# Optimization experiments

Measured on AMD Instinct MI355X. Metric: run time of the kernel, lower is better.

The kernel has to match this reference:

```python
import jax, jax.numpy as jnp
from jax import lax
import numpy as np


def tropical_conv1d(x, w, padding, mode):
    """Tropical semiring conv1d.
    y[b,o,t] = sum_c reduce_k ( x[b,c,t+k] + w[o,c,k] )
    where reduce is min (min-plus) or max (max-plus). Zero padding like nn.Conv1d.
    x: [B, C, L], w: [O, C, K] -> y: [B, O, L + 2p - K + 1]
    """
    if padding:
        x = jnp.pad(x, ((0, 0), (0, 0), (padding, padding)))
    B, C, L = x.shape
    O, _, K = w.shape
    Lo = L - K + 1
    big = jnp.array(np.inf if mode == 'min' else -np.inf, dtype=x.dtype)
    acc0 = jnp.full((B, O, C, Lo), big, dtype=x.dtype)
    red = jnp.minimum if mode == 'min' else jnp.maximum
    wk_all = jnp.moveaxis(w, 2, 0)          # [K, O, C]
    ks = jnp.arange(K)

    def step(acc, inp):
        k, wk = inp
        xs = lax.dynamic_slice_in_dim(x, k, Lo, axis=2)      # [B, C, Lo]
        v = xs[:, None, :, :] + wk[None, :, :, None]          # [B, O, C, Lo]
        return red(acc, v), None

    acc, _ = lax.scan(step, acc0, (ks, wk_all))
    return acc.sum(axis=2)                                    # [B, O, Lo]


def avg_pool1d_2(x):
    # avg_pool1d(kernel=2, stride=2), truncating odd tail like torch
    B, C, L = x.shape
    Lh = L // 2
    return x[..., : Lh * 2].reshape(B, C, Lh, 2).mean(axis=-1)


def setup_inputs() -> dict:
    key = jax.random.key(0)
    ks = jax.random.split(key, 9)
    B, Cin, L = 64, 3, 8192
    linear_size = 32448
    s = lambda k, shape, fan: jax.random.normal(k, shape, dtype=jnp.float32) * (1.0 / np.sqrt(fan))
    return {
        'input': jax.random.normal(ks[0], (B, Cin, L), dtype=jnp.float32),
        'w1': s(ks[1], (6, Cin, 80), Cin * 80),
        'w2': s(ks[2], (16, 6, 3), 6 * 3),
        'fc1_w': s(ks[3], (120, linear_size), linear_size),
        'fc1_b': jnp.zeros((120,), jnp.float32),
        'fc2_w': s(ks[4], (84, 120), 120),
        'fc2_b': jnp.zeros((84,), jnp.float32),
        'fc3_w': s(ks[5], (10, 84), 84),
        'fc3_b': jnp.zeros((10,), jnp.float32),
    }


def reference(input, w1, w2, fc1_w, fc1_b, fc2_w, fc2_b, fc3_w, fc3_b):
    x = tropical_conv1d(input, w1, padding=2, mode='min')   # [B,6,L-75]
    x = avg_pool1d_2(x)
    x = tropical_conv1d(x, w2, padding=0, mode='max')       # [B,16,L2]
    x = avg_pool1d_2(x)
    x = x.reshape(x.shape[0], -1)                            # [B, 16*floor(L2/2)]
    x = jax.nn.relu(x @ fc1_w.T + fc1_b)
    x = jax.nn.relu(x @ fc2_w.T + fc2_b)
    return x @ fc3_w.T + fc3_b
```

## Files before the change

### kernel.cpp

```cpp
#include <hip/hip_runtime.h>

#define BB 64
#define C1 3
#define LIN 8192
#define PAD1 2
#define O1 6
#define KK1 80
#define LP1 4058

#define O2 16
#define KK2 3
#define LP2 2028

#define NFLAT 32448
#define H1 120
#define H2 84
#define NOUT 10

typedef _Float16 h2 __attribute__((ext_vector_type(2)));
typedef _Float16 f16x8 __attribute__((ext_vector_type(8)));
typedef float f32x4 __attribute__((ext_vector_type(4)));
#define BIGH ((_Float16)30000.0f)

__global__ __launch_bounds__(256) void k_prep(const float* __restrict__ w1,
                                              float* __restrict__ whb) {
  const int idx = threadIdx.x + blockIdx.x * 256;
  if (idx >= (O1 * C1) * (KK1 / 2)) return;
  const int oc = idx / (KK1 / 2);
  const int m  = idx - oc * (KK1 / 2);
  h2 v;
  v.x = (_Float16)w1[oc * KK1 + 2 * m];
  v.y = (_Float16)w1[oc * KK1 + 2 * m + 1];
  whb[idx] = __builtin_bit_cast(float, v);
}

#define TJ1 256
#define NT1 16
#define DW1 298

__global__ __launch_bounds__(256) void k_conv1(const float* __restrict__ x,
                                               const float* __restrict__ whb,
                                               float* __restrict__ p1) {
  __shared__ float AB[C1][2 * DW1 + 2];
  const int b    = blockIdx.x >> 4;
  const int tile = blockIdx.x & 15;
  const int j0   = tile * TJ1;
  const int T0   = 2 * j0;
  const int tid  = threadIdx.x;

  for (int q = tid; q < C1 * DW1; q += 256) {
    const int c = q / DW1;
    const int d = q - c * DW1;
    const int E = T0 + 2 * d - PAD1;
    const float* xc = x + ((size_t)b * C1 + c) * LIN;
    float f0 = 0.f, f1 = 0.f, f2 = 0.f;
    if ((unsigned)E < LIN) f0 = xc[E];
    if ((unsigned)(E + 1) < LIN) f1 = xc[E + 1];
    if ((unsigned)(E + 2) < LIN) f2 = xc[E + 2];
    h2 A; A.x = (_Float16)f0; A.y = (_Float16)f1;
    h2 Bv; Bv.x = (_Float16)f1; Bv.y = (_Float16)f2;
    AB[c][2 * d]     = __builtin_bit_cast(float, A);
    AB[c][2 * d + 1] = __builtin_bit_cast(float, Bv);
  }
  __syncthreads();

  const int jj = tid;
  const int j  = j0 + jj;

  float s0 = 0.f, s1 = 0.f, s2 = 0.f, s3 = 0.f, s4 = 0.f, s5 = 0.f;

#pragma unroll
  for (int c = 0; c < C1; ++c) {
    h2 aA[O1], aB[O1];
#pragma unroll
    for (int o = 0; o < O1; ++o) {
      aA[o].x = BIGH; aA[o].y = BIGH;
      aB[o].x = BIGH; aB[o].y = BIGH;
    }
#pragma unroll 4
    for (int m = 0; m < KK1 / 2; ++m) {
      float2 v = *(const float2*)&AB[c][2 * (jj + m)];
      h2 Ad = __builtin_bit_cast(h2, v.x);
      h2 Bd = __builtin_bit_cast(h2, v.y);
#pragma unroll
      for (int o = 0; o < O1; ++o) {
        h2 W = __builtin_bit_cast(h2, whb[(o * C1 + c) * (KK1 / 2) + m]);
        aA[o] = __builtin_elementwise_min(aA[o], Ad + W);
        aB[o] = __builtin_elementwise_min(aB[o], Bd + W);
      }
    }
    float r[O1];
#pragma unroll
    for (int o = 0; o < O1; ++o)
      r[o] = fminf((float)aA[o].x, (float)aA[o].y) + fminf((float)aB[o].x, (float)aB[o].y);
    s0 += r[0]; s1 += r[1]; s2 += r[2]; s3 += r[3]; s4 += r[4]; s5 += r[5];
  }
  if (j < LP1) {
    float* pb = p1 + (size_t)b * O1 * LP1 + j;
    pb[0 * LP1] = 0.5f * s0;
    pb[1 * LP1] = 0.5f * s1;
    pb[2 * LP1] = 0.5f * s2;
    pb[3 * LP1] = 0.5f * s3;
    pb[4 * LP1] = 0.5f * s4;
    pb[5 * LP1] = 0.5f * s5;
  }
}

#define T2 256
#define XT2 516

__global__ __launch_bounds__(256) void k_conv2(const float* __restrict__ p1,
                                               const float* __restrict__ w2,
                                               _Float16* __restrict__ p2h) {
  __shared__ float ps[O1][XT2];
  __shared__ float w2s[O2 * O1 * KK2];
  const int b    = blockIdx.x >> 3;
  const int tile = blockIdx.x & 7;
  const int j0   = tile * T2;
  const int tid  = threadIdx.x;

  for (int idx = tid; idx < O2 * O1 * KK2; idx += 256) w2s[idx] = w2[idx];
  for (int idx = tid; idx < O1 * XT2; idx += 256) {
    int c = idx / XT2;
    int p = idx - c * XT2;
    int t = 2 * j0 + p;
    ps[c][p] = (t < LP1) ? p1[((size_t)b * O1 + c) * LP1 + t] : 0.f;
  }
  __syncthreads();

  const int j = j0 + tid;
  if (j >= LP2) return;
  const int lb = 2 * tid;
  float xv[O1][4];
#pragma unroll
  for (int c = 0; c < O1; ++c) {
    xv[c][0] = ps[c][lb];     xv[c][1] = ps[c][lb + 1];
    xv[c][2] = ps[c][lb + 2]; xv[c][3] = ps[c][lb + 3];
  }
#pragma unroll
  for (int o = 0; o < O2; ++o) {
    float s = 0.f;
#pragma unroll
    for (int c = 0; c < O1; ++c) {
      float w0  = w2s[(o * O1 + c) * KK2 + 0];
      float w1v = w2s[(o * O1 + c) * KK2 + 1];
      float w2v = w2s[(o * O1 + c) * KK2 + 2];
      float m0 = fmaxf(fmaxf(xv[c][0] + w0, xv[c][1] + w1v), xv[c][2] + w2v);
      float m1 = fmaxf(fmaxf(xv[c][1] + w0, xv[c][2] + w1v), xv[c][3] + w2v);
      s += m0 + m1;
    }
    p2h[(size_t)b * NFLAT + o * LP2 + j] = (_Float16)(0.5f * s);
  }
}

#define KC2 64
#define NKC2 507

__global__ __launch_bounds__(256) void k_fc1(const _Float16* __restrict__ p2h,
                                             const float* __restrict__ w,
                                             _Float16* __restrict__ part) {
  __shared__ _Float16 bs[64][KC2];
  const int kc  = blockIdx.x;
  const int k0  = kc * KC2;
  const int tid = threadIdx.x;

#pragma unroll
  for (int r = 0; r < 2; ++r) {
    const int task = tid + 256 * r;
    const int row  = task >> 3;
    const int c4   = task & 7;
    float4 v = *(const float4*)&p2h[(size_t)row * NFLAT + k0 + c4 * 8];
    *(float4*)&bs[row][c4 * 8] = v;
  }
  __syncthreads();

  const int lane = tid & 63;
  const int wid  = tid >> 6;
  const int m_l  = lane & 15;
  const int q    = lane >> 4;
  const int m0   = wid * 32;

  const int rowA0 = m0 + m_l;
  int rowA1 = m0 + 16 + m_l;
  if (rowA1 > H1 - 1) rowA1 = H1 - 1;
  const float* wp0 = w + (size_t)rowA0 * NFLAT + k0 + q * 8;
  const float* wp1 = w + (size_t)rowA1 * NFLAT + k0 + q * 8;

  f32x4 acc[2][4];
#pragma unroll
  for (int t = 0; t < 2; ++t)
#pragma unroll
    for (int nt = 0; nt < 4; ++nt) acc[t][nt] = (f32x4){0.f, 0.f, 0.f, 0.f};

#pragma unroll
  for (int ks = 0; ks < 2; ++ks) {
    float4 a0l = *(const float4*)(wp0 + ks * 32);
    float4 a0h = *(const float4*)(wp0 + ks * 32 + 4);
    float4 a1l = *(const float4*)(wp1 + ks * 32);
    float4 a1h = *(const float4*)(wp1 + ks * 32 + 4);
    f16x8 A0, A1;
    A0[0] = (_Float16)a0l.x; A0[1] = (_Float16)a0l.y;
    A0[2] = (_Float16)a0l.z; A0[3] = (_Float16)a0l.w;
    A0[4] = (_Float16)a0h.x; A0[5] = (_Float16)a0h.y;
    A0[6] = (_Float16)a0h.z; A0[7] = (_Float16)a0h.w;
    A1[0] = (_Float16)a1l.x; A1[1] = (_Float16)a1l.y;
    A1[2] = (_Float16)a1l.z; A1[3] = (_Float16)a1l.w;
    A1[4] = (_Float16)a1h.x; A1[5] = (_Float16)a1h.y;
    A1[6] = (_Float16)a1h.z; A1[7] = (_Float16)a1h.w;
#pragma unroll
    for (int nt = 0; nt < 4; ++nt) {
      f16x8 Bf = *(const f16x8*)&bs[nt * 16 + m_l][ks * 32 + q * 8];
      acc[0][nt] = __builtin_amdgcn_mfma_f32_16x16x32_f16(A0, Bf, acc[0][nt], 0, 0, 0);
      acc[1][nt] = __builtin_amdgcn_mfma_f32_16x16x32_f16(A1, Bf, acc[1][nt], 0, 0, 0);
    }
  }

#pragma unroll
  for (int t = 0; t < 2; ++t)
#pragma unroll
    for (int nt = 0; nt < 4; ++nt)
#pragma unroll
      for (int r = 0; r < 4; ++r) {
        const int i = m0 + t * 16 + q * 4 + r;
        if (i < H1)
          part[((size_t)kc * H1 + i) * 64 + nt * 16 + m_l] = (_Float16)acc[t][nt][r];
      }
}

__global__ __launch_bounds__(512) void k_fc1red(const _Float16* __restrict__ part,
                                                float* __restrict__ part2) {
  __shared__ float red[512];
  const int bx  = blockIdx.x;
  const int s   = bx / H1;
  const int i   = bx - s * H1;
  const int tid = threadIdx.x;
  const int b   = tid & 63;
  const int sub = tid >> 6;
  const int kc0 = s * 127;
  const int kc1 = (kc0 + 127 < NKC2) ? kc0 + 127 : NKC2;
  float acc = 0.f;
  for (int kc = kc0 + sub; kc < kc1; kc += 8)
    acc += (float)part[((size_t)kc * H1 + i) * 64 + b];
  red[tid] = acc;
  __syncthreads();
  if (tid < 64) {
    float t = 0.f;
#pragma unroll
    for (int s2 = 0; s2 < 8; ++s2) t += red[b + 64 * s2];
    part2[((size_t)s * H1 + i) * 64 + b] = t;
  }
}

__global__ __launch_bounds__(128) void k_head(const float* __restrict__ part2,
                                              const float* __restrict__ fc1_b,
                                              const float* __restrict__ fc2_w,
                                              const float* __restrict__ fc2_b,
                                              const float* __restrict__ fc3_w,
                                              const float* __restrict__ fc3_b,
                                              float* __restrict__ out) {
  __shared__ float h1s[H1];
  __shared__ float h2s[H2];
  const int b = blockIdx.x;
  const int tid = threadIdx.x;
  if (tid < H1) {
    float v = part2[((size_t)0 * H1 + tid) * 64 + b]
            + part2[((size_t)1 * H1 + tid) * 64 + b]
            + part2[((size_t)2 * H1 + tid) * 64 + b]
            + part2[((size_t)3 * H1 + tid) * 64 + b];
    h1s[tid] = fmaxf(v + fc1_b[tid], 0.f);
  }
  __syncthreads();
  if (tid < H2) {
    float s = fc2_b[tid];
#pragma unroll 4
    for (int n = 0; n < H1; ++n) s += h1s[n] * fc2_w[tid * H1 + n];
    h2s[tid] = fmaxf(s, 0.f);
  }
  __syncthreads();
  if (tid < NOUT) {
    float s = fc3_b[tid];
#pragma unroll 4
    for (int n = 0; n < H2; ++n) s += h2s[n] * fc3_w[tid * H2 + n];
    out[b * NOUT + tid] = s;
  }
}

extern "C" void kernel_launch(void* const* d_in, const int* in_sizes, int n_in,
                              void* d_out, int out_size, void* d_ws, size_t ws_size,
                              hipStream_t stream) {
  const float* x     = (const float*)d_in[0];
  const float* w1    = (const float*)d_in[1];
  const float* w2    = (const float*)d_in[2];
  const float* fc1_w = (const float*)d_in[3];
  const float* fc1_b = (const float*)d_in[4];
  const float* fc2_w = (const float*)d_in[5];
  const float* fc2_b = (const float*)d_in[6];
  const float* fc3_w = (const float*)d_in[7];
  const float* fc3_b = (const float*)d_in[8];

  float* ws = (float*)d_ws;
  float*     p1    = ws;
  _Float16*  p2h   = (_Float16*)(p1 + (size_t)BB * O1 * LP1);
  _Float16*  part  = p2h + (size_t)BB * NFLAT;
  float*     part2 = (float*)(part + (size_t)NKC2 * H1 * 64);
  float*     whb   = part2 + (size_t)4 * H1 * 64;
  float*     out   = (float*)d_out;

  hipLaunchKernelGGL(k_prep, dim3(3), dim3(256), 0, stream, w1, whb);
  hipLaunchKernelGGL(k_conv1, dim3(BB * NT1), dim3(256), 0, stream, x, whb, p1);
  hipLaunchKernelGGL(k_conv2, dim3(BB * 8), dim3(256), 0, stream, p1, w2, p2h);
  hipLaunchKernelGGL(k_fc1, dim3(NKC2), dim3(256), 0, stream, p2h, fc1_w, part);
  hipLaunchKernelGGL(k_fc1red, dim3(4 * H1), dim3(512), 0, stream, part, part2);
  hipLaunchKernelGGL(k_head, dim3(BB), dim3(128), 0, stream, part2, fc1_b, fc2_w, fc2_b,
                     fc3_w, fc3_b, out);
}
```

Measured before the change: 144.0 us.

## Register-block conv1 to two outputs per thread with shared-memory weights

The first tropical conv kernel doubles its tile so each thread computes two output positions 256 apart. Each weight fetch is now reused across both positions, and the weights are staged in shared memory and read as float4. The input window is split into separate A/B shared arrays so four taps can be loaded with one vector read. In exchange the grid has half as many blocks and register pressure is higher, and the float4 LDS reads use thread-dependent offsets that may not be 16-byte aligned.

```diff
diff --git a/kernel.cpp b/kernel.cpp
--- a/kernel.cpp
+++ b/kernel.cpp
@@ -21,6 +21,8 @@
 typedef _Float16 f16x8 __attribute__((ext_vector_type(8)));
 typedef float f32x4 __attribute__((ext_vector_type(4)));
 #define BIGH ((_Float16)30000.0f)
+
+__device__ __forceinline__ h2 bch2(float f) { return __builtin_bit_cast(h2, f); }
 
 __global__ __launch_bounds__(256) void k_prep(const float* __restrict__ w1,
                                               float* __restrict__ whb) {
@@ -34,24 +36,27 @@
   whb[idx] = __builtin_bit_cast(float, v);
 }
 
-#define TJ1 256
-#define NT1 16
-#define DW1 298
+#define TJ1 512
+#define NT1 8
+#define DWIN 552
+#define DPAD 556
 
 __global__ __launch_bounds__(256) void k_conv1(const float* __restrict__ x,
                                                const float* __restrict__ whb,
                                                float* __restrict__ p1) {
-  __shared__ float AB[C1][2 * DW1 + 2];
-  const int b    = blockIdx.x >> 4;
-  const int tile = blockIdx.x & 15;
+  __shared__ float As[C1][DPAD];
+  __shared__ float Bs[C1][DPAD];
+  __shared__ float ws[O1 * C1 * 40];
+  const int b    = blockIdx.x >> 3;
+  const int tile = blockIdx.x & 7;
   const int j0   = tile * TJ1;
-  const int T0   = 2 * j0;
   const int tid  = threadIdx.x;
 
-  for (int q = tid; q < C1 * DW1; q += 256) {
-    const int c = q / DW1;
-    const int d = q - c * DW1;
-    const int E = T0 + 2 * d - PAD1;
+  for (int idx = tid; idx < O1 * C1 * 40; idx += 256) ws[idx] = whb[idx];
+  for (int q = tid; q < C1 * DWIN; q += 256) {
+    const int c = q / DWIN;
+    const int d = q - c * DWIN;
+    const int E = 2 * (j0 + d) - PAD1;
     const float* xc = x + ((size_t)b * C1 + c) * LIN;
     float f0 = 0.f, f1 = 0.f, f2 = 0.f;
     if ((unsigned)E < LIN) f0 = xc[E];
@@ -59,50 +64,74 @@
     if ((unsigned)(E + 2) < LIN) f2 = xc[E + 2];
     h2 A; A.x = (_Float16)f0; A.y = (_Float16)f1;
     h2 Bv; Bv.x = (_Float16)f1; Bv.y = (_Float16)f2;
-    AB[c][2 * d]     = __builtin_bit_cast(float, A);
-    AB[c][2 * d + 1] = __builtin_bit_cast(float, Bv);
+    As[c][d] = __builtin_bit_cast(float, A);
+    Bs[c][d] = __builtin_bit_cast(float, Bv);
   }
   __syncthreads();
 
   const int jj = tid;
-  const int j  = j0 + jj;
-
-  float s0 = 0.f, s1 = 0.f, s2 = 0.f, s3 = 0.f, s4 = 0.f, s5 = 0.f;
-
-#pragma unroll
+  float r1[O1] = {0.f, 0.f, 0.f, 0.f, 0.f, 0.f};
+  float r2[O1] = {0.f, 0.f, 0.f, 0.f, 0.f, 0.f};
+
   for (int c = 0; c < C1; ++c) {
-    h2 aA[O1], aB[O1];
+    h2 a1A[O1], a1B[O1], a2A[O1], a2B[O1];
 #pragma unroll
     for (int o = 0; o < O1; ++o) {
-      aA[o].x = BIGH; aA[o].y = BIGH;
-      aB[o].x = BIGH; aB[o].y = BIGH;
-    }
-#pragma unroll 4
-    for (int m = 0; m < KK1 / 2; ++m) {
-      float2 v = *(const float2*)&AB[c][2 * (jj + m)];
-      h2 Ad = __builtin_bit_cast(h2, v.x);
-      h2 Bd = __builtin_bit_cast(h2, v.y);
+      a1A[o].x = BIGH; a1A[o].y = BIGH;  a1B[o].x = BIGH; a1B[o].y = BIGH;
+      a2A[o].x = BIGH; a2A[o].y = BIGH;  a2B[o].x = BIGH; a2B[o].y = BIGH;
+    }
+#pragma unroll 2
+    for (int mq = 0; mq < 10; ++mq) {
+      float4 xa1 = *(const float4*)&As[c][jj + 4 * mq];
+      float4 xb1 = *(const float4*)&Bs[c][jj + 4 * mq];
+      float4 xa2 = *(const float4*)&As[c][jj + 256 + 4 * mq];
+      float4 xb2 = *(const float4*)&Bs[c][jj + 256 + 4 * mq];
+      h2 A10 = bch2(xa1.x), A11 = bch2(xa1.y), A12 = bch2(xa1.z), A13 = bch2(xa1.w);
+      h2 B10 = bch2(xb1.x), B11 = bch2(xb1.y), B12 = bch2(xb1.z), B13 = bch2(xb1.w);
+      h2 A20 = bch2(xa2.x), A21 = bch2(xa2.y), A22 = bch2(xa2.z), A23 = bch2(xa2.w);
+      h2 B20 = bch2(xb2.x), B21 = bch2(xb2.y), B22 = bch2(xb2.z), B23 = bch2(xb2.w);
 #pragma unroll
       for (int o = 0; o < O1; ++o) {
-        h2 W = __builtin_bit_cast(h2, whb[(o * C1 + c) * (KK1 / 2) + m]);
-        aA[o] = __builtin_elementwise_min(aA[o], Ad + W);
-        aB[o] = __builtin_elementwise_min(aB[o], Bd + W);
+        float4 wq = *(const float4*)&ws[(o * C1 + c) * 40 + 4 * mq];
+        h2 w0 = bch2(wq.x), w1v = bch2(wq.y), w2v = bch2(wq.z), w3v = bch2(wq.w);
+        a1A[o] = __builtin_elementwise_min(a1A[o], A10 + w0);
+        a1B[o] = __builtin_elementwise_min(a1B[o], B10 + w0);
+        a1A[o] = __builtin_elementwise_min(a1A[o], A11 + w1v);
+        a1B[o] = __builtin_elementwise_min(a1B[o], B11 + w1v);
+        a1A[o] = __builtin_elementwise_min(a1A[o], A12 + w2v);
+        a1B[o] = __builtin_elementwise_min(a1B[o], B12 + w2v);
+        a1A[o] = __builtin_elementwise_min(a1A[o], A13 + w3v);
+        a1B[o] = __builtin_elementwise_min(a1B[o], B13 + w3v);
+        a2A[o] = __builtin_elementwise_min(a2A[o], A20 + w0);
+        a2B[o] = __builtin_elementwise_min(a2B[o], B20 + w0);
+        a2A[o] = __builtin_elementwise_min(a2A[o], A21 + w1v);
+        a2B[o] = __builtin_elementwise_min(a2B[o], B21 + w1v);
+        a2A[o] = __builtin_elementwise_min(a2A[o], A22 + w2v);
+        a2B[o] = __builtin_elementwise_min(a2B[o], B22 + w2v);
+        a2A[o] = __builtin_elementwise_min(a2A[o], A23 + w3v);
+        a2B[o] = __builtin_elementwise_min(a2B[o], B23 + w3v);
       }
     }
-    float r[O1];
-#pragma unroll
-    for (int o = 0; o < O1; ++o)
-      r[o] = fminf((float)aA[o].x, (float)aA[o].y) + fminf((float)aB[o].x, (float)aB[o].y);
-    s0 += r[0]; s1 += r[1]; s2 += r[2]; s3 += r[3]; s4 += r[4]; s5 += r[5];
-  }
-  if (j < LP1) {
-    float* pb = p1 + (size_t)b * O1 * LP1 + j;
-    pb[0 * LP1] = 0.5f * s0;
-    pb[1 * LP1] = 0.5f * s1;
-    pb[2 * LP1] = 0.5f * s2;
-    pb[3 * LP1] = 0.5f * s3;
-    pb[4 * LP1] = 0.5f * s4;
-    pb[5 * LP1] = 0.5f * s5;
+#pragma unroll
+    for (int o = 0; o < O1; ++o) {
+      r1[o] += fminf((float)a1A[o].x, (float)a1A[o].y) +
+               fminf((float)a1B[o].x, (float)a1B[o].y);
+      r2[o] += fminf((float)a2A[o].x, (float)a2A[o].y) +
+               fminf((float)a2B[o].x, (float)a2B[o].y);
+    }
+  }
+
+  const int j1 = j0 + jj;
+  const int j2 = j0 + 256 + jj;
+  if (j1 < LP1) {
+    float* pb = p1 + (size_t)b * O1 * LP1 + j1;
+#pragma unroll
+    for (int o = 0; o < O1; ++o) pb[o * LP1] = 0.5f * r1[o];
+  }
+  if (j2 < LP1) {
+    float* pb = p1 + (size_t)b * O1 * LP1 + j2;
+#pragma unroll
+    for (int o = 0; o < O1; ++o) pb[o * LP1] = 0.5f * r2[o];
   }
 }
 
```

After: 148.7 us. +3.3%, slower.

## Restructure conv1 to split output channels across threads and stage weights in LDS

Applied to the files above, without the earlier changes.

The conv1 kernel now uses 512 threads per block, with each half computing three of the six output channels for the same positions. The shifted B operand is built in registers by bit-shuffling adjacent packed halves, so only the A windows are stored in shared memory. Weights are copied to LDS and read as float4, and input windows are read as float4 with a rolling register. The aim is to cut LDS footprint and global weight loads and to raise occupancy, at the cost of the extra shuffle ALU work and of loading the input tile redundantly for both channel groups.

```diff
diff --git a/kernel.cpp b/kernel.cpp
--- a/kernel.cpp
+++ b/kernel.cpp
@@ -21,6 +21,13 @@
 typedef _Float16 f16x8 __attribute__((ext_vector_type(8)));
 typedef float f32x4 __attribute__((ext_vector_type(4)));
 #define BIGH ((_Float16)30000.0f)
+
+__device__ __forceinline__ h2 bch2(float f) { return __builtin_bit_cast(h2, f); }
+__device__ __forceinline__ h2 mkB(float nxt, float cur) {
+  unsigned lo = __builtin_bit_cast(unsigned, cur);
+  unsigned hi = __builtin_bit_cast(unsigned, nxt);
+  return __builtin_bit_cast(h2, (lo >> 16) | (hi << 16));
+}
 
 __global__ __launch_bounds__(256) void k_prep(const float* __restrict__ w1,
                                               float* __restrict__ whb) {
@@ -36,73 +43,81 @@
 
 #define TJ1 256
 #define NT1 16
-#define DW1 298
-
-__global__ __launch_bounds__(256) void k_conv1(const float* __restrict__ x,
-                                               const float* __restrict__ whb,
-                                               float* __restrict__ p1) {
-  __shared__ float AB[C1][2 * DW1 + 2];
+#define DWIN 297
+#define DPAD 304
+
+__global__ __launch_bounds__(512, 8) void k_conv1(const float* __restrict__ x,
+                                                  const float* __restrict__ whb,
+                                                  float* __restrict__ p1) {
+  __shared__ float As[C1][DPAD];
+  __shared__ float ws[O1 * C1 * 40];
   const int b    = blockIdx.x >> 4;
   const int tile = blockIdx.x & 15;
   const int j0   = tile * TJ1;
-  const int T0   = 2 * j0;
   const int tid  = threadIdx.x;
 
-  for (int q = tid; q < C1 * DW1; q += 256) {
-    const int c = q / DW1;
-    const int d = q - c * DW1;
-    const int E = T0 + 2 * d - PAD1;
+  for (int idx = tid; idx < O1 * C1 * 40; idx += 512) ws[idx] = whb[idx];
+  for (int q = tid; q < C1 * DWIN; q += 512) {
+    const int c = q / DWIN;
+    const int d = q - c * DWIN;
+    const int E = 2 * (j0 + d) - PAD1;
     const float* xc = x + ((size_t)b * C1 + c) * LIN;
-    float f0 = 0.f, f1 = 0.f, f2 = 0.f;
+    float f0 = 0.f, f1 = 0.f;
     if ((unsigned)E < LIN) f0 = xc[E];
     if ((unsigned)(E + 1) < LIN) f1 = xc[E + 1];
-    if ((unsigned)(E + 2) < LIN) f2 = xc[E + 2];
     h2 A; A.x = (_Float16)f0; A.y = (_Float16)f1;
-    h2 Bv; Bv.x = (_Float16)f1; Bv.y = (_Float16)f2;
-    AB[c][2 * d]     = __builtin_bit_cast(float, A);
-    AB[c][2 * d + 1] = __builtin_bit_cast(float, Bv);
-  }
-  __syncthreads();
-
-  const int jj = tid;
-  const int j  = j0 + jj;
-
-  float s0 = 0.f, s1 = 0.f, s2 = 0.f, s3 = 0.f, s4 = 0.f, s5 = 0.f;
-
-#pragma unroll
+    As[c][d] = __builtin_bit_cast(float, A);
+  }
+  __syncthreads();
+
+  const int og = tid >> 8;
+  const int jj = tid & 255;
+  const int ob = og * 3;
+
+  float r0 = 0.f, r1 = 0.f, r2 = 0.f;
+
   for (int c = 0; c < C1; ++c) {
-    h2 aA[O1], aB[O1];
-#pragma unroll
-    for (int o = 0; o < O1; ++o) {
-      aA[o].x = BIGH; aA[o].y = BIGH;
-      aB[o].x = BIGH; aB[o].y = BIGH;
+    h2 aA[3], aB[3];
+#pragma unroll
+    for (int oo = 0; oo < 3; ++oo) {
+      aA[oo].x = BIGH; aA[oo].y = BIGH;
+      aB[oo].x = BIGH; aB[oo].y = BIGH;
     }
-#pragma unroll 4
-    for (int m = 0; m < KK1 / 2; ++m) {
-      float2 v = *(const float2*)&AB[c][2 * (jj + m)];
-      h2 Ad = __builtin_bit_cast(h2, v.x);
-      h2 Bd = __builtin_bit_cast(h2, v.y);
-#pragma unroll
-      for (int o = 0; o < O1; ++o) {
-        h2 W = __builtin_bit_cast(h2, whb[(o * C1 + c) * (KK1 / 2) + m]);
-        aA[o] = __builtin_elementwise_min(aA[o], Ad + W);
-        aB[o] = __builtin_elementwise_min(aB[o], Bd + W);
+    float4 cur = *(const float4*)&As[c][jj];
+#pragma unroll 2
+    for (int mq = 0; mq < 10; ++mq) {
+      float4 nxt = *(const float4*)&As[c][jj + 4 * mq + 4];
+      h2 A0 = bch2(cur.x), A1 = bch2(cur.y), A2 = bch2(cur.z), A3 = bch2(cur.w);
+      h2 B0 = mkB(cur.y, cur.x);
+      h2 B1 = mkB(cur.z, cur.y);
+      h2 B2 = mkB(cur.w, cur.z);
+      h2 B3 = mkB(nxt.x, cur.w);
+#pragma unroll
+      for (int oo = 0; oo < 3; ++oo) {
+        float4 wq = *(const float4*)&ws[((ob + oo) * C1 + c) * 40 + 4 * mq];
+        h2 w0 = bch2(wq.x), w1v = bch2(wq.y), w2v = bch2(wq.z), w3v = bch2(wq.w);
+        aA[oo] = __builtin_elementwise_min(aA[oo], A0 + w0);
+        aB[oo] = __builtin_elementwise_min(aB[oo], B0 + w0);
+        aA[oo] = __builtin_elementwise_min(aA[oo], A1 + w1v);
+        aB[oo] = __builtin_elementwise_min(aB[oo], B1 + w1v);
+        aA[oo] = __builtin_elementwise_min(aA[oo], A2 + w2v);
+        aB[oo] = __builtin_elementwise_min(aB[oo], B2 + w2v);
+        aA[oo] = __builtin_elementwise_min(aA[oo], A3 + w3v);
+        aB[oo] = __builtin_elementwise_min(aB[oo], B3 + w3v);
       }
+      cur = nxt;
     }
-    float r[O1];
-#pragma unroll
-    for (int o = 0; o < O1; ++o)
-      r[o] = fminf((float)aA[o].x, (float)aA[o].y) + fminf((float)aB[o].x, (float)aB[o].y);
-    s0 += r[0]; s1 += r[1]; s2 += r[2]; s3 += r[3]; s4 += r[4]; s5 += r[5];
-  }
+    r0 += fminf((float)aA[0].x, (float)aA[0].y) + fminf((float)aB[0].x, (float)aB[0].y);
+    r1 += fminf((float)aA[1].x, (float)aA[1].y) + fminf((float)aB[1].x, (float)aB[1].y);
+    r2 += fminf((float)aA[2].x, (float)aA[2].y) + fminf((float)aB[2].x, (float)aB[2].y);
+  }
+
+  const int j = j0 + jj;
   if (j < LP1) {
     float* pb = p1 + (size_t)b * O1 * LP1 + j;
-    pb[0 * LP1] = 0.5f * s0;
-    pb[1 * LP1] = 0.5f * s1;
-    pb[2 * LP1] = 0.5f * s2;
-    pb[3 * LP1] = 0.5f * s3;
-    pb[4 * LP1] = 0.5f * s4;
-    pb[5 * LP1] = 0.5f * s5;
+    pb[(ob + 0) * LP1] = 0.5f * r0;
+    pb[(ob + 1) * LP1] = 0.5f * r1;
+    pb[(ob + 2) * LP1] = 0.5f * r2;
   }
 }
 
@@ -307,7 +322,7 @@
   float*     out   = (float*)d_out;
 
   hipLaunchKernelGGL(k_prep, dim3(3), dim3(256), 0, stream, w1, whb);
-  hipLaunchKernelGGL(k_conv1, dim3(BB * NT1), dim3(256), 0, stream, x, whb, p1);
+  hipLaunchKernelGGL(k_conv1, dim3(BB * NT1), dim3(512), 0, stream, x, whb, p1);
   hipLaunchKernelGGL(k_conv2, dim3(BB * 8), dim3(256), 0, stream, p1, w2, p2h);
   hipLaunchKernelGGL(k_fc1, dim3(NKC2), dim3(256), 0, stream, p2h, fc1_w, part);
   hipLaunchKernelGGL(k_fc1red, dim3(4 * H1), dim3(512), 0, stream, part, part2);
```

Measured after the change: 146.5 us. No clear change (+1.8%).
